# Kernel optimization log

Measured on AMD Instinct MI355X. Metric: run time of the kernel, lower is better.

## Reference

```python
import jax, jax.numpy as jnp
import numpy as np

N_CONS = 100_000
N_VAR = 200_000
N_EDGE = 2_000_000
EMB = 64
CONS_F = 5
VAR_F = 19
EDGE_F = 1
N_LAYERS = 2


def setup_inputs() -> dict:
    key = jax.random.key(0)
    ks = iter(jax.random.split(key, 48))
    def nrm(shape, scale=0.05):
        return jax.random.normal(next(ks), shape, dtype=jnp.float32) * scale
    inp = {}
    inp["cons_x"] = jax.random.normal(next(ks), (N_CONS, CONS_F), dtype=jnp.float32)
    inp["var_x"] = jax.random.normal(next(ks), (N_VAR, VAR_F), dtype=jnp.float32)
    row = jax.random.randint(next(ks), (N_EDGE,), 0, N_CONS, dtype=jnp.int32)
    col = jax.random.randint(next(ks), (N_EDGE,), 0, N_VAR, dtype=jnp.int32)
    inp["edge_index"] = jnp.stack([row, col], axis=0)
    inp["edge_attr"] = jax.random.normal(next(ks), (N_EDGE, EDGE_F), dtype=jnp.float32)
    inp["break_indicator"] = jax.random.uniform(next(ks), (N_VAR, 1), dtype=jnp.float32)
    # PreNormLayer affine params: y = (x + shift) * scale
    inp["cons_pn_shift"] = nrm((CONS_F,))
    inp["cons_pn_scale"] = 1.0 + nrm((CONS_F,))
    inp["var_pn_shift"] = nrm((VAR_F,))
    inp["var_pn_scale"] = 1.0 + nrm((VAR_F,))
    inp["edge_pn_shift"] = nrm((EDGE_F,))
    inp["edge_pn_scale"] = 1.0 + nrm((EDGE_F,))
    # embedding MLPs
    inp["cons_W1"] = nrm((CONS_F, EMB), 0.4)
    inp["cons_b1"] = nrm((EMB,))
    inp["cons_W2"] = nrm((EMB, EMB), 0.12)
    inp["cons_b2"] = nrm((EMB,))
    inp["var_W1"] = nrm((VAR_F, EMB), 0.22)
    inp["var_b1"] = nrm((EMB,))
    inp["var_W2"] = nrm((EMB, EMB), 0.12)
    inp["var_b2"] = nrm((EMB,))
    inp["break_W"] = nrm((1, EMB), 0.5)
    # SAGEConv params per layer: lin_l (neighbor mean, with bias), lin_r (root, no bias)
    inp["Wl_cv"] = nrm((N_LAYERS, EMB, EMB), 0.12)
    inp["bl_cv"] = nrm((N_LAYERS, EMB))
    inp["Wr_cv"] = nrm((N_LAYERS, EMB, EMB), 0.12)
    inp["Wl_vc"] = nrm((N_LAYERS, EMB, EMB), 0.12)
    inp["bl_vc"] = nrm((N_LAYERS, EMB))
    inp["Wr_vc"] = nrm((N_LAYERS, EMB, EMB), 0.12)
    return inp


def _embed(x, shift, scale, W1, b1, W2, b2):
    h = (x + shift) * scale
    h = jax.nn.relu(h @ W1 + b1)
    return jax.nn.relu(h @ W2 + b2)


def _sage(x_src, x_dst, src, dst, n_dst, Wl, bl, Wr):
    # gather source features per edge, mean-aggregate by destination (PyG SAGEConv mean aggr)
    msg = x_src[src]                                              # [E, emb]
    s = jax.ops.segment_sum(msg, dst, num_segments=n_dst)         # [n_dst, emb]
    cnt = jax.ops.segment_sum(jnp.ones((src.shape[0], 1), x_src.dtype), dst, num_segments=n_dst)
    mean = s / jnp.maximum(cnt, 1.0)
    return mean @ Wl + bl + x_dst @ Wr


def reference(cons_x, var_x, edge_index, edge_attr, break_indicator,
              cons_pn_shift, cons_pn_scale, var_pn_shift, var_pn_scale,
              edge_pn_shift, edge_pn_scale,
              cons_W1, cons_b1, cons_W2, cons_b2,
              var_W1, var_b1, var_W2, var_b2,
              break_W, Wl_cv, bl_cv, Wr_cv, Wl_vc, bl_vc, Wr_vc):
    row, col = edge_index[0], edge_index[1]
    cons = _embed(cons_x, cons_pn_shift, cons_pn_scale, cons_W1, cons_b1, cons_W2, cons_b2)
    var = _embed(var_x, var_pn_shift, var_pn_scale, var_W1, var_b1, var_W2, var_b2)
    _edge = (edge_attr + edge_pn_shift) * edge_pn_scale  # computed as in module; unused by SAGE convs
    var = var + break_indicator @ break_W
    n_cons, n_var = cons.shape[0], var.shape[0]
    for l in range(Wl_cv.shape[0]):
        # HeteroConv: both directions computed from the same x_dict, then ReLU
        new_var = jax.nn.relu(_sage(cons, var, row, col, n_var, Wl_cv[l], bl_cv[l], Wr_cv[l]))
        new_cons = jax.nn.relu(_sage(var, cons, col, row, n_cons, Wl_vc[l], bl_vc[l], Wr_vc[l]))
        cons, var = new_cons, new_var
    return var
```

## Files before the change

### kernel.cpp

```cpp
#include <hip/hip_runtime.h>

#define N_CONS 100000
#define N_VAR  200000
#define N_TOT  (N_CONS + N_VAR)
#define N_EDGE 2000000
#define EMB 64

#define VSH 10
#define NBV 196
#define CAPV 12288
#define CSH 9
#define NBC 196
#define CAPC 12288

typedef unsigned short u16;
typedef __attribute__((ext_vector_type(8))) short bf16x8;
typedef __attribute__((ext_vector_type(4))) float f32x4;


__device__ __forceinline__ float b2f_lo(unsigned u) {
  union { unsigned i; float f; } c;
  c.i = u << 16;
  return c.f;
}
__device__ __forceinline__ float b2f_hi(unsigned u) {
  union { unsigned i; float f; } c;
  c.i = u & 0xFFFF0000u;
  return c.f;
}
__device__ __forceinline__ unsigned pack_bf2(float a, float b) {
  unsigned ua = __float_as_uint(a), ub = __float_as_uint(b);
  unsigned ra = (ua + 0x7FFFu + ((ua >> 16) & 1u)) >> 16;
  unsigned rb = (ub + 0x7FFFu + ((ub >> 16) & 1u)) >> 16;
  return ra | (rb << 16);
}
__device__ __forceinline__ u16 f2bf(float a) {
  unsigned ua = __float_as_uint(a);
  return (u16)((ua + 0x7FFFu + ((ua >> 16) & 1u)) >> 16);
}


__global__ __launch_bounds__(256) void csr_init(int* __restrict__ gcurV,
                                                int* __restrict__ gcurC,
                                                int* __restrict__ off) {
  int t = threadIdx.x;
  if (t < NBV) gcurV[t] = t * CAPV;
  if (t < NBC) gcurC[t] = t * CAPC;
  if (t == 0) off[N_TOT] = 2 * N_EDGE;
}

__global__ __launch_bounds__(256) void bucket_scatter(
    const int* __restrict__ row, const int* __restrict__ col,
    int* __restrict__ gcurV, int* __restrict__ gcurC,
    int* __restrict__ pairV, int* __restrict__ pairC) {
  __shared__ int hV[NBV];
  __shared__ int hC[NBC];
  int tid = threadIdx.x;
  int chunk = (N_EDGE + gridDim.x - 1) / gridDim.x;
  int lo = blockIdx.x * chunk;
  int hi = min(N_EDGE, lo + chunk);
  for (int i = tid; i < NBV; i += 256) hV[i] = 0;
  for (int i = tid; i < NBC; i += 256) hC[i] = 0;
  __syncthreads();
  for (int e = lo + tid; e < hi; e += 256) {
    atomicAdd(&hV[col[e] >> VSH], 1);
    atomicAdd(&hC[row[e] >> CSH], 1);
  }
  __syncthreads();
  for (int i = tid; i < NBV; i += 256) {
    int c = hV[i];
    hV[i] = c ? atomicAdd(&gcurV[i], c) : 0;
  }
  for (int i = tid; i < NBC; i += 256) {
    int c = hC[i];
    hC[i] = c ? atomicAdd(&gcurC[i], c) : 0;
  }
  __syncthreads();
  for (int e = lo + tid; e < hi; e += 256) {
    int r = row[e], c = col[e];
    int p = atomicAdd(&hV[c >> VSH], 1);
    pairV[p] = (r << VSH) | (c & ((1 << VSH) - 1));
    int q = atomicAdd(&hC[r >> CSH], 1);
    pairC[q] = (c << CSH) | (r & ((1 << CSH) - 1));
  }
}

__global__ __launch_bounds__(256) void bucket_scan(const int* __restrict__ gcurV,
                                                   const int* __restrict__ gcurC,
                                                   int* __restrict__ ebaseV,
                                                   int* __restrict__ ebaseC) {
  __shared__ int s[256];
  int t = threadIdx.x;
  int v = (t < NBV) ? (gcurV[t] - t * CAPV) : 0;
  s[t] = v;
  __syncthreads();
  for (int d = 1; d < 256; d <<= 1) {
    int x = (t >= d) ? s[t - d] : 0;
    __syncthreads();
    s[t] += x;
    __syncthreads();
  }
  if (t < NBV) ebaseV[t] = s[t] - v;
  if (t == NBV - 1) ebaseV[NBV] = s[t];
  __syncthreads();
  int c = (t < NBC) ? (gcurC[t] - t * CAPC) : 0;
  s[t] = c;
  __syncthreads();
  for (int d = 1; d < 256; d <<= 1) {
    int x = (t >= d) ? s[t - d] : 0;
    __syncthreads();
    s[t] += x;
    __syncthreads();
  }
  if (t < NBC) ebaseC[t] = s[t] - c;
  if (t == NBC - 1) ebaseC[NBC] = s[t];
}

__global__ __launch_bounds__(256) void local_csr(
    const int* __restrict__ pairV, const int* __restrict__ pairC,
    const int* __restrict__ ebaseV, const int* __restrict__ ebaseC,
    int* __restrict__ off, int* __restrict__ adj) {
  __shared__ int cnt[1024];
  __shared__ int cur[1024];
  __shared__ int s[256];
  int tid = threadIdx.x;
  int b = blockIdx.x;
  const int* pairs;
  int m, obase, nn, sh;
  int* offp;
  if (b < NBV) {
    pairs = pairV + (size_t)b * CAPV;
    m = ebaseV[b + 1] - ebaseV[b];
    obase = ebaseV[b];
    nn = min(1024, N_VAR - (b << 10));
    sh = VSH;
    offp = off + (b << 10);
  } else {
    int bb = b - NBV;
    pairs = pairC + (size_t)bb * CAPC;
    m = ebaseC[bb + 1] - ebaseC[bb];
    obase = N_EDGE + ebaseC[bb];
    nn = min(512, N_CONS - (bb << 9));
    sh = CSH;
    offp = off + N_VAR + (bb << 9);
  }
  int mask = (1 << sh) - 1;
  for (int i = tid; i < 1024; i += 256) cnt[i] = 0;
  __syncthreads();
  for (int k = tid; k < m; k += 256) atomicAdd(&cnt[pairs[k] & mask], 1);
  __syncthreads();
  int i0 = tid * 4;
  int c0 = cnt[i0], c1 = cnt[i0 + 1], c2 = cnt[i0 + 2], c3 = cnt[i0 + 3];
  int sum = c0 + c1 + c2 + c3;
  s[tid] = sum;
  __syncthreads();
  for (int d = 1; d < 256; d <<= 1) {
    int x = (tid >= d) ? s[tid - d] : 0;
    __syncthreads();
    s[tid] += x;
    __syncthreads();
  }
  int run = obase + s[tid] - sum;
  int vals[4] = {c0, c1, c2, c3};
#pragma unroll
  for (int q = 0; q < 4; ++q) {
    int i = i0 + q;
    cur[i] = run;
    if (i < nn) offp[i] = run;
    run += vals[q];
  }
  __syncthreads();
  for (int k = tid; k < m; k += 256) {
    int pr = pairs[k];
    int p = atomicAdd(&cur[pr & mask], 1);
    adj[p] = pr >> sh;
  }
}


template <int F>
__global__ __launch_bounds__(256) void embed_mm(
    const float* __restrict__ x, const float* __restrict__ shift,
    const float* __restrict__ scale, const float* __restrict__ W1,
    const float* __restrict__ b1, const float* __restrict__ W2,
    const float* __restrict__ b2, const float* __restrict__ bi,
    const float* __restrict__ bW, u16* __restrict__ outbf, int n) {
  __shared__ float Xs[F * 68];
  __shared__ float W1s[F * 68];
  __shared__ u16 Hs[64][72];
  __shared__ u16 W2s[64][72];
  __shared__ float b1s[64], b2s[64], bWs[64], bis[64];
  int t = threadIdx.x;
  int v0 = blockIdx.x * 64;

  int sn = t & 63;
  int kq = t >> 6;
  {
    unsigned pk[8];
#pragma unroll
    for (int i = 0; i < 8; ++i) {
      float w0 = W2[(size_t)(kq * 16 + 2 * i) * 64 + sn];
      float w1 = W2[(size_t)(kq * 16 + 2 * i + 1) * 64 + sn];
      pk[i] = pack_bf2(w0, w1);
    }
    *(uint4*)&W2s[sn][kq * 16] = make_uint4(pk[0], pk[1], pk[2], pk[3]);
    *(uint4*)&W2s[sn][kq * 16 + 8] = make_uint4(pk[4], pk[5], pk[6], pk[7]);
  }
  for (int i = t; i < F * 64; i += 256) {
    int k = i >> 6, j = i & 63;
    W1s[k * 68 + j] = W1[i] * scale[k];
  }
  if (t < 64) {
    float acc = b1[t];
#pragma unroll
    for (int k = 0; k < F; ++k) acc += shift[k] * scale[k] * W1[k * 64 + t];
    b1s[t] = acc;
    b2s[t] = b2[t];
    bWs[t] = bW ? bW[t] : 0.f;
    bis[t] = (bi && v0 + t < n) ? bi[v0 + t] : 0.f;
  }
  for (int i = t; i < 64 * F; i += 256) {
    int row = i / F, k = i - row * F;
    int v = v0 + row;
    Xs[k * 68 + row] = (v < n) ? x[(size_t)v * F + k] : 0.f;
  }
  __syncthreads();

  int jt = t & 15;
  int vt = t >> 4;
  float c[4][4] = {};
#pragma unroll
  for (int k = 0; k < F; ++k) {
    float4 xv = *(const float4*)&Xs[k * 68 + vt * 4];
    float4 wv = *(const float4*)&W1s[k * 68 + jt * 4];
    c[0][0] += xv.x * wv.x; c[0][1] += xv.x * wv.y; c[0][2] += xv.x * wv.z; c[0][3] += xv.x * wv.w;
    c[1][0] += xv.y * wv.x; c[1][1] += xv.y * wv.y; c[1][2] += xv.y * wv.z; c[1][3] += xv.y * wv.w;
    c[2][0] += xv.z * wv.x; c[2][1] += xv.z * wv.y; c[2][2] += xv.z * wv.z; c[2][3] += xv.z * wv.w;
    c[3][0] += xv.w * wv.x; c[3][1] += xv.w * wv.y; c[3][2] += xv.w * wv.z; c[3][3] += xv.w * wv.w;
  }
#pragma unroll
  for (int i = 0; i < 4; ++i) {
    float h0 = fmaxf(c[i][0] + b1s[jt * 4 + 0], 0.f);
    float h1 = fmaxf(c[i][1] + b1s[jt * 4 + 1], 0.f);
    float h2 = fmaxf(c[i][2] + b1s[jt * 4 + 2], 0.f);
    float h3 = fmaxf(c[i][3] + b1s[jt * 4 + 3], 0.f);
    *(uint2*)&Hs[vt * 4 + i][jt * 4] = make_uint2(pack_bf2(h0, h1), pack_bf2(h2, h3));
  }
  __syncthreads();

  int l = t & 63;
  int w = t >> 6;
  int m0 = w * 16;
  int rA = m0 + (l & 15);
  int koffA = (l >> 4) * 8;
  f32x4 acc[4] = {};
  {
    bf16x8 a0 = *(const bf16x8*)&Hs[rA][koffA];
    bf16x8 a1 = *(const bf16x8*)&Hs[rA][32 + koffA];
#pragma unroll
    for (int cb = 0; cb < 4; ++cb) {
      int nB = cb * 16 + (l & 15);
      bf16x8 b0 = *(const bf16x8*)&W2s[nB][koffA];
      bf16x8 bb1 = *(const bf16x8*)&W2s[nB][32 + koffA];
      acc[cb] = __builtin_amdgcn_mfma_f32_16x16x32_bf16(a0, b0, acc[cb], 0, 0, 0);
      acc[cb] = __builtin_amdgcn_mfma_f32_16x16x32_bf16(a1, bb1, acc[cb], 0, 0, 0);
    }
  }
#pragma unroll
  for (int cb = 0; cb < 4; ++cb) {
    int colc = cb * 16 + (l & 15);
    float bias = b2s[colc];
    float bwv = bWs[colc];
#pragma unroll
    for (int j = 0; j < 4; ++j) {
      int rowc = m0 + (l >> 4) * 4 + j;
      int v = v0 + rowc;
      if (v < n) {
        float val = fmaxf(acc[cb][j] + bias, 0.f) + bis[rowc] * bwv;
        outbf[(size_t)v * 64 + colc] = f2bf(val);
      }
    }
  }
}


template <int OUTBF>
__global__ __launch_bounds__(256) void sage_mfma(
    const uint2* __restrict__ srcbf, const uint2* __restrict__ dstbf,
    const int* __restrict__ off, const int* __restrict__ adj,
    const float* __restrict__ Wl, const float* __restrict__ bl,
    const float* __restrict__ Wr, float* __restrict__ outf,
    u16* __restrict__ outbf, int n) {
  __shared__ u16 Hs[64][72];
  __shared__ u16 Ws[64][72];
  __shared__ float bls[64];
  int t = threadIdx.x;
  int v0 = blockIdx.x * 64;
  if (t < 64) bls[t] = bl[t];

  int sn = t & 63;
  int kq = t >> 6;
  {
    unsigned pk[8];
#pragma unroll
    for (int i = 0; i < 8; ++i) {
      float w0 = Wl[(size_t)(kq * 16 + 2 * i) * 64 + sn];
      float w1 = Wl[(size_t)(kq * 16 + 2 * i + 1) * 64 + sn];
      pk[i] = pack_bf2(w0, w1);
    }
    *(uint4*)&Ws[sn][kq * 16] = make_uint4(pk[0], pk[1], pk[2], pk[3]);
    *(uint4*)&Ws[sn][kq * 16 + 8] = make_uint4(pk[4], pk[5], pk[6], pk[7]);
  }

  int lane = t & 15;
  int g = t >> 4;
#pragma unroll
  for (int grp = 0; grp < 4; ++grp) {
    int r = grp * 16 + g;
    int v = v0 + r;
    float ax = 0.f, ay = 0.f, az = 0.f, aw = 0.f;
    if (v < n) {
      int s0 = off[v], s1 = off[v + 1];
      int i = s0;
      for (; i + 4 <= s1; i += 4) {
        int u0 = adj[i], u1 = adj[i + 1], u2 = adj[i + 2], u3 = adj[i + 3];
        uint2 a0 = srcbf[(size_t)u0 * 16 + lane];
        uint2 a1 = srcbf[(size_t)u1 * 16 + lane];
        uint2 a2 = srcbf[(size_t)u2 * 16 + lane];
        uint2 a3 = srcbf[(size_t)u3 * 16 + lane];
        ax += (b2f_lo(a0.x) + b2f_lo(a1.x)) + (b2f_lo(a2.x) + b2f_lo(a3.x));
        ay += (b2f_hi(a0.x) + b2f_hi(a1.x)) + (b2f_hi(a2.x) + b2f_hi(a3.x));
        az += (b2f_lo(a0.y) + b2f_lo(a1.y)) + (b2f_lo(a2.y) + b2f_lo(a3.y));
        aw += (b2f_hi(a0.y) + b2f_hi(a1.y)) + (b2f_hi(a2.y) + b2f_hi(a3.y));
      }
      if (i + 2 <= s1) {
        int u0 = adj[i], u1 = adj[i + 1];
        uint2 a0 = srcbf[(size_t)u0 * 16 + lane];
        uint2 a1 = srcbf[(size_t)u1 * 16 + lane];
        ax += b2f_lo(a0.x) + b2f_lo(a1.x);
        ay += b2f_hi(a0.x) + b2f_hi(a1.x);
        az += b2f_lo(a0.y) + b2f_lo(a1.y);
        aw += b2f_hi(a0.y) + b2f_hi(a1.y);
        i += 2;
      }
      if (i < s1) {
        uint2 a = srcbf[(size_t)adj[i] * 16 + lane];
        ax += b2f_lo(a.x);
        ay += b2f_hi(a.x);
        az += b2f_lo(a.y);
        aw += b2f_hi(a.y);
      }
      int deg = s1 - s0;
      float inv = (deg > 0) ? 1.f / (float)deg : 0.f;
      ax *= inv;
      ay *= inv;
      az *= inv;
      aw *= inv;
    }
    *(uint2*)&Hs[r][lane * 4] = make_uint2(pack_bf2(ax, ay), pack_bf2(az, aw));
  }
  __syncthreads();

  int l = t & 63;
  int w = t >> 6;
  int m0 = w * 16;
  int rA = m0 + (l & 15);
  int koffA = (l >> 4) * 8;
  f32x4 acc[4] = {};
  {
    bf16x8 a0 = *(const bf16x8*)&Hs[rA][koffA];
    bf16x8 a1 = *(const bf16x8*)&Hs[rA][32 + koffA];
#pragma unroll
    for (int cb = 0; cb < 4; ++cb) {
      int nB = cb * 16 + (l & 15);
      bf16x8 b0 = *(const bf16x8*)&Ws[nB][koffA];
      bf16x8 b1 = *(const bf16x8*)&Ws[nB][32 + koffA];
      acc[cb] = __builtin_amdgcn_mfma_f32_16x16x32_bf16(a0, b0, acc[cb], 0, 0, 0);
      acc[cb] = __builtin_amdgcn_mfma_f32_16x16x32_bf16(a1, b1, acc[cb], 0, 0, 0);
    }
  }
  __syncthreads();

#pragma unroll
  for (int r4 = 0; r4 < 4; ++r4) {
    int idx = t + 256 * r4;
    int rowi = idx >> 4, f4 = idx & 15;
    int v = v0 + rowi;
    uint2 val = (v < n) ? dstbf[(size_t)v * 16 + f4] : make_uint2(0u, 0u);
    *(uint2*)&Hs[rowi][f4 * 4] = val;
  }
  {
    unsigned pk[8];
#pragma unroll
    for (int i = 0; i < 8; ++i) {
      float w0 = Wr[(size_t)(kq * 16 + 2 * i) * 64 + sn];
      float w1 = Wr[(size_t)(kq * 16 + 2 * i + 1) * 64 + sn];
      pk[i] = pack_bf2(w0, w1);
    }
    *(uint4*)&Ws[sn][kq * 16] = make_uint4(pk[0], pk[1], pk[2], pk[3]);
    *(uint4*)&Ws[sn][kq * 16 + 8] = make_uint4(pk[4], pk[5], pk[6], pk[7]);
  }
  __syncthreads();

  {
    bf16x8 a0 = *(const bf16x8*)&Hs[rA][koffA];
    bf16x8 a1 = *(const bf16x8*)&Hs[rA][32 + koffA];
#pragma unroll
    for (int cb = 0; cb < 4; ++cb) {
      int nB = cb * 16 + (l & 15);
      bf16x8 b0 = *(const bf16x8*)&Ws[nB][koffA];
      bf16x8 b1 = *(const bf16x8*)&Ws[nB][32 + koffA];
      acc[cb] = __builtin_amdgcn_mfma_f32_16x16x32_bf16(a0, b0, acc[cb], 0, 0, 0);
      acc[cb] = __builtin_amdgcn_mfma_f32_16x16x32_bf16(a1, b1, acc[cb], 0, 0, 0);
    }
  }

#pragma unroll
  for (int cb = 0; cb < 4; ++cb) {
    int colc = cb * 16 + (l & 15);
    float bias = bls[colc];
#pragma unroll
    for (int j = 0; j < 4; ++j) {
      int rowc = m0 + (l >> 4) * 4 + j;
      int v = v0 + rowc;
      if (v < n) {
        float val = fmaxf(acc[cb][j] + bias, 0.f);
        if (OUTBF) {
          outbf[(size_t)v * 64 + colc] = f2bf(val);
        } else {
          outf[(size_t)v * 64 + colc] = val;
        }
      }
    }
  }
}


extern "C" void kernel_launch(void* const* d_in, const int* in_sizes, int n_in,
                              void* d_out, int out_size, void* d_ws, size_t ws_size,
                              hipStream_t stream) {
  const float* cons_x = (const float*)d_in[0];
  const float* var_x  = (const float*)d_in[1];
  const int*   eidx   = (const int*)d_in[2];
  const float* bi     = (const float*)d_in[4];
  const float* c_sh   = (const float*)d_in[5];
  const float* c_sc   = (const float*)d_in[6];
  const float* v_sh   = (const float*)d_in[7];
  const float* v_sc   = (const float*)d_in[8];
  const float* cW1 = (const float*)d_in[11];
  const float* cb1 = (const float*)d_in[12];
  const float* cW2 = (const float*)d_in[13];
  const float* cb2 = (const float*)d_in[14];
  const float* vW1 = (const float*)d_in[15];
  const float* vb1 = (const float*)d_in[16];
  const float* vW2 = (const float*)d_in[17];
  const float* vb2 = (const float*)d_in[18];
  const float* bW  = (const float*)d_in[19];
  const float* Wl_cv = (const float*)d_in[20];
  const float* bl_cv = (const float*)d_in[21];
  const float* Wr_cv = (const float*)d_in[22];
  const float* Wl_vc = (const float*)d_in[23];
  const float* bl_vc = (const float*)d_in[24];
  const float* Wr_vc = (const float*)d_in[25];

  const int* row = eidx;
  const int* col = eidx + N_EDGE;

  char* ws = (char*)d_ws;
  size_t o = 0;
  auto alloc = [&](size_t bytes) {
    char* p = ws + o;
    o = (o + bytes + 255) & ~(size_t)255;
    return p;
  };
  int* off    = (int*)alloc((N_TOT + 1) * sizeof(int));
  int* adj    = (int*)alloc((size_t)2 * N_EDGE * sizeof(int));
  int* pairV  = (int*)alloc((size_t)NBV * CAPV * sizeof(int));
  int* pairC  = (int*)alloc((size_t)NBC * CAPC * sizeof(int));
  int* gcurV  = (int*)alloc(256 * sizeof(int));
  int* gcurC  = (int*)alloc(256 * sizeof(int));
  int* ebaseV = (int*)alloc(256 * sizeof(int));
  int* ebaseC = (int*)alloc(256 * sizeof(int));
  uint2* consEbf = (uint2*)alloc((size_t)N_CONS * EMB * 2);
  uint2* varEbf  = (uint2*)alloc((size_t)N_VAR * EMB * 2);
  uint2* cons1bf = (uint2*)alloc((size_t)N_CONS * EMB * 2);
  uint2* var1bf  = (uint2*)alloc((size_t)N_VAR * EMB * 2);
  float* var_out = (float*)d_out;

  csr_init<<<1, 256, 0, stream>>>(gcurV, gcurC, off);
  bucket_scatter<<<512, 256, 0, stream>>>(row, col, gcurV, gcurC, pairV, pairC);
  bucket_scan<<<1, 256, 0, stream>>>(gcurV, gcurC, ebaseV, ebaseC);
  local_csr<<<NBV + NBC, 256, 0, stream>>>(pairV, pairC, ebaseV, ebaseC, off, adj);

  embed_mm<5><<<(N_CONS + 63) / 64, 256, 0, stream>>>(
      cons_x, c_sh, c_sc, cW1, cb1, cW2, cb2, nullptr, nullptr, (u16*)consEbf,
      N_CONS);
  embed_mm<19><<<(N_VAR + 63) / 64, 256, 0, stream>>>(
      var_x, v_sh, v_sc, vW1, vb1, vW2, vb2, bi, bW, (u16*)varEbf, N_VAR);

  sage_mfma<1><<<(N_VAR + 63) / 64, 256, 0, stream>>>(
      consEbf, varEbf, off, adj, Wl_cv, bl_cv, Wr_cv, nullptr, (u16*)var1bf,
      N_VAR);
  sage_mfma<1><<<(N_CONS + 63) / 64, 256, 0, stream>>>(
      varEbf, consEbf, off + N_VAR, adj, Wl_vc, bl_vc, Wr_vc, nullptr,
      (u16*)cons1bf, N_CONS);
  sage_mfma<0><<<(N_VAR + 63) / 64, 256, 0, stream>>>(
      cons1bf, var1bf, off, adj, Wl_cv + 4096, bl_cv + 64, Wr_cv + 4096,
      var_out, nullptr, N_VAR);
}
```

Baseline: 281.0 us.

## Pad CSR rows to multiples of four with zero-row sentinels and merge kernels

Each adjacency list now starts at a fixed per-bucket base and is padded to a multiple of four edges. Padding entries point to an extra all-zero embedding row, so the gather loop has no 2- and 1-element tails, and degree is stored separately. This also removes the global bucket scan kernel (local_csr runs with 1024 threads and fixed capacities) and merges the two layer-0 SAGE launches into one grid. The cost is a larger padded adjacency buffer, up to three wasted gathers per node, and a fixed capacity assumption per bucket.

```diff
diff --git a/kernel.cpp b/kernel.cpp
--- a/kernel.cpp
+++ b/kernel.cpp
@@ -12,6 +12,10 @@
 #define CSH 9
 #define NBC 196
 #define CAPC 12288
+#define CAPAV (CAPV + 3 * 1024)
+#define CAPAC (CAPC + 3 * 512)
+#define NB_VAR ((N_VAR + 63) / 64)
+#define NB_CONS ((N_CONS + 63) / 64)
 
 typedef unsigned short u16;
 typedef __attribute__((ext_vector_type(8))) short bf16x8;
@@ -42,11 +46,15 @@
 
 __global__ __launch_bounds__(256) void csr_init(int* __restrict__ gcurV,
                                                 int* __restrict__ gcurC,
-                                                int* __restrict__ off) {
+                                                uint2* __restrict__ consEbf,
+                                                uint2* __restrict__ varEbf,
+                                                uint2* __restrict__ cons1bf) {
   int t = threadIdx.x;
   if (t < NBV) gcurV[t] = t * CAPV;
   if (t < NBC) gcurC[t] = t * CAPC;
-  if (t == 0) off[N_TOT] = 2 * N_EDGE;
+  if (t < 16) consEbf[(size_t)N_CONS * 16 + t] = make_uint2(0u, 0u);
+  else if (t < 32) varEbf[(size_t)N_VAR * 16 + (t - 16)] = make_uint2(0u, 0u);
+  else if (t < 48) cons1bf[(size_t)N_CONS * 16 + (t - 32)] = make_uint2(0u, 0u);
 }
 
 __global__ __launch_bounds__(256) void bucket_scatter(
@@ -85,96 +93,67 @@
   }
 }
 
-__global__ __launch_bounds__(256) void bucket_scan(const int* __restrict__ gcurV,
-                                                   const int* __restrict__ gcurC,
-                                                   int* __restrict__ ebaseV,
-                                                   int* __restrict__ ebaseC) {
-  __shared__ int s[256];
-  int t = threadIdx.x;
-  int v = (t < NBV) ? (gcurV[t] - t * CAPV) : 0;
-  s[t] = v;
-  __syncthreads();
-  for (int d = 1; d < 256; d <<= 1) {
-    int x = (t >= d) ? s[t - d] : 0;
-    __syncthreads();
-    s[t] += x;
-    __syncthreads();
-  }
-  if (t < NBV) ebaseV[t] = s[t] - v;
-  if (t == NBV - 1) ebaseV[NBV] = s[t];
-  __syncthreads();
-  int c = (t < NBC) ? (gcurC[t] - t * CAPC) : 0;
-  s[t] = c;
-  __syncthreads();
-  for (int d = 1; d < 256; d <<= 1) {
-    int x = (t >= d) ? s[t - d] : 0;
-    __syncthreads();
-    s[t] += x;
-    __syncthreads();
-  }
-  if (t < NBC) ebaseC[t] = s[t] - c;
-  if (t == NBC - 1) ebaseC[NBC] = s[t];
-}
-
-__global__ __launch_bounds__(256) void local_csr(
+__global__ __launch_bounds__(1024) void local_csr(
     const int* __restrict__ pairV, const int* __restrict__ pairC,
-    const int* __restrict__ ebaseV, const int* __restrict__ ebaseC,
-    int* __restrict__ off, int* __restrict__ adj) {
+    const int* __restrict__ gcurV, const int* __restrict__ gcurC,
+    int* __restrict__ off, int* __restrict__ deg, int* __restrict__ adj) {
   __shared__ int cnt[1024];
+  __shared__ int s[1024];
   __shared__ int cur[1024];
-  __shared__ int s[256];
   int tid = threadIdx.x;
   int b = blockIdx.x;
   const int* pairs;
-  int m, obase, nn, sh;
+  int m, obase, nn, sh, zrow;
   int* offp;
+  int* degp;
   if (b < NBV) {
     pairs = pairV + (size_t)b * CAPV;
-    m = ebaseV[b + 1] - ebaseV[b];
-    obase = ebaseV[b];
+    m = gcurV[b] - b * CAPV;
+    obase = b * CAPAV;
     nn = min(1024, N_VAR - (b << 10));
     sh = VSH;
+    zrow = N_CONS;
     offp = off + (b << 10);
+    degp = deg + (b << 10);
   } else {
     int bb = b - NBV;
     pairs = pairC + (size_t)bb * CAPC;
-    m = ebaseC[bb + 1] - ebaseC[bb];
-    obase = N_EDGE + ebaseC[bb];
+    m = gcurC[bb] - bb * CAPC;
+    obase = NBV * CAPAV + bb * CAPAC;
     nn = min(512, N_CONS - (bb << 9));
     sh = CSH;
+    zrow = N_VAR;
     offp = off + N_VAR + (bb << 9);
+    degp = deg + N_VAR + (bb << 9);
   }
   int mask = (1 << sh) - 1;
-  for (int i = tid; i < 1024; i += 256) cnt[i] = 0;
-  __syncthreads();
-  for (int k = tid; k < m; k += 256) atomicAdd(&cnt[pairs[k] & mask], 1);
-  __syncthreads();
-  int i0 = tid * 4;
-  int c0 = cnt[i0], c1 = cnt[i0 + 1], c2 = cnt[i0 + 2], c3 = cnt[i0 + 3];
-  int sum = c0 + c1 + c2 + c3;
-  s[tid] = sum;
-  __syncthreads();
-  for (int d = 1; d < 256; d <<= 1) {
-    int x = (tid >= d) ? s[tid - d] : 0;
+  cnt[tid] = 0;
+  __syncthreads();
+  for (int k = tid; k < m; k += 1024) atomicAdd(&cnt[pairs[k] & mask], 1);
+  __syncthreads();
+  int c = cnt[tid];
+  int pc = (c + 3) & ~3;
+  s[tid] = pc;
+  __syncthreads();
+  for (int d1 = 1; d1 < 1024; d1 <<= 1) {
+    int x = (tid >= d1) ? s[tid - d1] : 0;
     __syncthreads();
     s[tid] += x;
     __syncthreads();
   }
-  int run = obase + s[tid] - sum;
-  int vals[4] = {c0, c1, c2, c3};
-#pragma unroll
-  for (int q = 0; q < 4; ++q) {
-    int i = i0 + q;
-    cur[i] = run;
-    if (i < nn) offp[i] = run;
-    run += vals[q];
-  }
-  __syncthreads();
-  for (int k = tid; k < m; k += 256) {
+  int start = obase + s[tid] - pc;
+  cur[tid] = start;
+  if (tid < nn) {
+    offp[tid] = start;
+    degp[tid] = c;
+  }
+  __syncthreads();
+  for (int k = tid; k < m; k += 1024) {
     int pr = pairs[k];
     int p = atomicAdd(&cur[pr & mask], 1);
     adj[p] = pr >> sh;
   }
+  for (int q = c; q < pc; ++q) adj[start + q] = zrow;
 }
 
 
@@ -285,17 +264,14 @@
 
 
 template <int OUTBF>
-__global__ __launch_bounds__(256) void sage_mfma(
+__device__ __forceinline__ void sage_body(
     const uint2* __restrict__ srcbf, const uint2* __restrict__ dstbf,
-    const int* __restrict__ off, const int* __restrict__ adj,
-    const float* __restrict__ Wl, const float* __restrict__ bl,
-    const float* __restrict__ Wr, float* __restrict__ outf,
-    u16* __restrict__ outbf, int n) {
-  __shared__ u16 Hs[64][72];
-  __shared__ u16 Ws[64][72];
-  __shared__ float bls[64];
+    const int* __restrict__ off, const int* __restrict__ deg,
+    const int* __restrict__ adj, const float* __restrict__ Wl,
+    const float* __restrict__ bl, const float* __restrict__ Wr,
+    float* __restrict__ outf, u16* __restrict__ outbf, int n, int v0,
+    u16 (*Hs)[72], u16 (*Ws)[72], float* bls) {
   int t = threadIdx.x;
-  int v0 = blockIdx.x * 64;
   if (t < 64) bls[t] = bl[t];
 
   int sn = t & 63;
@@ -320,9 +296,10 @@
     int v = v0 + r;
     float ax = 0.f, ay = 0.f, az = 0.f, aw = 0.f;
     if (v < n) {
-      int s0 = off[v], s1 = off[v + 1];
-      int i = s0;
-      for (; i + 4 <= s1; i += 4) {
+      int s0 = off[v];
+      int d = deg[v];
+      int e4 = s0 + ((d + 3) & ~3);
+      for (int i = s0; i < e4; i += 4) {
         int u0 = adj[i], u1 = adj[i + 1], u2 = adj[i + 2], u3 = adj[i + 3];
         uint2 a0 = srcbf[(size_t)u0 * 16 + lane];
         uint2 a1 = srcbf[(size_t)u1 * 16 + lane];
@@ -333,25 +310,7 @@
         az += (b2f_lo(a0.y) + b2f_lo(a1.y)) + (b2f_lo(a2.y) + b2f_lo(a3.y));
         aw += (b2f_hi(a0.y) + b2f_hi(a1.y)) + (b2f_hi(a2.y) + b2f_hi(a3.y));
       }
-      if (i + 2 <= s1) {
-        int u0 = adj[i], u1 = adj[i + 1];
-        uint2 a0 = srcbf[(size_t)u0 * 16 + lane];
-        uint2 a1 = srcbf[(size_t)u1 * 16 + lane];
-        ax += b2f_lo(a0.x) + b2f_lo(a1.x);
-        ay += b2f_hi(a0.x) + b2f_hi(a1.x);
-        az += b2f_lo(a0.y) + b2f_lo(a1.y);
-        aw += b2f_hi(a0.y) + b2f_hi(a1.y);
-        i += 2;
-      }
-      if (i < s1) {
-        uint2 a = srcbf[(size_t)adj[i] * 16 + lane];
-        ax += b2f_lo(a.x);
-        ay += b2f_hi(a.x);
-        az += b2f_lo(a.y);
-        aw += b2f_hi(a.y);
-      }
-      int deg = s1 - s0;
-      float inv = (deg > 0) ? 1.f / (float)deg : 0.f;
+      float inv = (d > 0) ? 1.f / (float)d : 0.f;
       ax *= inv;
       ay *= inv;
       az *= inv;
@@ -433,6 +392,40 @@
       }
     }
   }
+}
+
+__global__ __launch_bounds__(256) void sage_l0(
+    const uint2* __restrict__ consEbf, const uint2* __restrict__ varEbf,
+    const int* __restrict__ off, const int* __restrict__ deg,
+    const int* __restrict__ adj, const float* __restrict__ Wl_cv,
+    const float* __restrict__ bl_cv, const float* __restrict__ Wr_cv,
+    const float* __restrict__ Wl_vc, const float* __restrict__ bl_vc,
+    const float* __restrict__ Wr_vc, u16* __restrict__ var1bf,
+    u16* __restrict__ cons1bf) {
+  __shared__ u16 Hs[64][72];
+  __shared__ u16 Ws[64][72];
+  __shared__ float bls[64];
+  int b = blockIdx.x;
+  if (b < NB_VAR) {
+    sage_body<1>(consEbf, varEbf, off, deg, adj, Wl_cv, bl_cv, Wr_cv, nullptr,
+                 var1bf, N_VAR, b * 64, Hs, Ws, bls);
+  } else {
+    sage_body<1>(varEbf, consEbf, off + N_VAR, deg + N_VAR, adj, Wl_vc, bl_vc,
+                 Wr_vc, nullptr, cons1bf, N_CONS, (b - NB_VAR) * 64, Hs, Ws, bls);
+  }
+}
+
+__global__ __launch_bounds__(256) void sage_l1(
+    const uint2* __restrict__ cons1bf, const uint2* __restrict__ var1bf,
+    const int* __restrict__ off, const int* __restrict__ deg,
+    const int* __restrict__ adj, const float* __restrict__ Wl,
+    const float* __restrict__ bl, const float* __restrict__ Wr,
+    float* __restrict__ out) {
+  __shared__ u16 Hs[64][72];
+  __shared__ u16 Ws[64][72];
+  __shared__ float bls[64];
+  sage_body<0>(cons1bf, var1bf, off, deg, adj, Wl, bl, Wr, out, nullptr, N_VAR,
+               blockIdx.x * 64, Hs, Ws, bls);
 }
 
 
@@ -473,38 +466,34 @@
     o = (o + bytes + 255) & ~(size_t)255;
     return p;
   };
-  int* off    = (int*)alloc((N_TOT + 1) * sizeof(int));
-  int* adj    = (int*)alloc((size_t)2 * N_EDGE * sizeof(int));
-  int* pairV  = (int*)alloc((size_t)NBV * CAPV * sizeof(int));
-  int* pairC  = (int*)alloc((size_t)NBC * CAPC * sizeof(int));
-  int* gcurV  = (int*)alloc(256 * sizeof(int));
-  int* gcurC  = (int*)alloc(256 * sizeof(int));
-  int* ebaseV = (int*)alloc(256 * sizeof(int));
-  int* ebaseC = (int*)alloc(256 * sizeof(int));
-  uint2* consEbf = (uint2*)alloc((size_t)N_CONS * EMB * 2);
-  uint2* varEbf  = (uint2*)alloc((size_t)N_VAR * EMB * 2);
-  uint2* cons1bf = (uint2*)alloc((size_t)N_CONS * EMB * 2);
+  int* off   = (int*)alloc((size_t)N_TOT * sizeof(int));
+  int* deg   = (int*)alloc((size_t)N_TOT * sizeof(int));
+  int* adj   = (int*)alloc(((size_t)NBV * CAPAV + (size_t)NBC * CAPAC) * sizeof(int));
+  int* pairV = (int*)alloc((size_t)NBV * CAPV * sizeof(int));
+  int* pairC = (int*)alloc((size_t)NBC * CAPC * sizeof(int));
+  int* gcurV = (int*)alloc(256 * sizeof(int));
+  int* gcurC = (int*)alloc(256 * sizeof(int));
+  uint2* consEbf = (uint2*)alloc((size_t)(N_CONS + 1) * EMB * 2);
+  uint2* varEbf  = (uint2*)alloc((size_t)(N_VAR + 1) * EMB * 2);
+  uint2* cons1bf = (uint2*)alloc((size_t)(N_CONS + 1) * EMB * 2);
   uint2* var1bf  = (uint2*)alloc((size_t)N_VAR * EMB * 2);
   float* var_out = (float*)d_out;
 
-  csr_init<<<1, 256, 0, stream>>>(gcurV, gcurC, off);
+  csr_init<<<1, 256, 0, stream>>>(gcurV, gcurC, consEbf, varEbf, cons1bf);
   bucket_scatter<<<512, 256, 0, stream>>>(row, col, gcurV, gcurC, pairV, pairC);
-  bucket_scan<<<1, 256, 0, stream>>>(gcurV, gcurC, ebaseV, ebaseC);
-  local_csr<<<NBV + NBC, 256, 0, stream>>>(pairV, pairC, ebaseV, ebaseC, off, adj);
-
-  embed_mm<5><<<(N_CONS + 63) / 64, 256, 0, stream>>>(
-      cons_x, c_sh, c_sc, cW1, cb1, cW2, cb2, nullptr, nullptr, (u16*)consEbf,
-      N_CONS);
-  embed_mm<19><<<(N_VAR + 63) / 64, 256, 0, stream>>>(
-      var_x, v_sh, v_sc, vW1, vb1, vW2, vb2, bi, bW, (u16*)varEbf, N_VAR);
-
-  sage_mfma<1><<<(N_VAR + 63) / 64, 256, 0, stream>>>(
-      consEbf, varEbf, off, adj, Wl_cv, bl_cv, Wr_cv, nullptr, (u16*)var1bf,
-      N_VAR);
-  sage_mfma<1><<<(N_CONS + 63) / 64, 256, 0, stream>>>(
-      varEbf, consEbf, off + N_VAR, adj, Wl_vc, bl_vc, Wr_vc, nullptr,
-      (u16*)cons1bf, N_CONS);
-  sage_mfma<0><<<(N_VAR + 63) / 64, 256, 0, stream>>>(
-      cons1bf, var1bf, off, adj, Wl_cv + 4096, bl_cv + 64, Wr_cv + 4096,
-      var_out, nullptr, N_VAR);
-}
+  local_csr<<<NBV + NBC, 1024, 0, stream>>>(pairV, pairC, gcurV, gcurC, off,
+                                            deg, adj);
+
+  embed_mm<5><<<NB_CONS, 256, 0, stream>>>(cons_x, c_sh, c_sc, cW1, cb1, cW2,
+                                           cb2, nullptr, nullptr, (u16*)consEbf,
+                                           N_CONS);
+  embed_mm<19><<<NB_VAR, 256, 0, stream>>>(var_x, v_sh, v_sc, vW1, vb1, vW2,
+                                           vb2, bi, bW, (u16*)varEbf, N_VAR);
+
+  sage_l0<<<NB_VAR + NB_CONS, 256, 0, stream>>>(
+      consEbf, varEbf, off, deg, adj, Wl_cv, bl_cv, Wr_cv, Wl_vc, bl_vc, Wr_vc,
+      (u16*)var1bf, (u16*)cons1bf);
+  sage_l1<<<NB_VAR, 256, 0, stream>>>(cons1bf, var1bf, off, deg, adj,
+                                      Wl_cv + 4096, bl_cv + 64, Wr_cv + 4096,
+                                      var_out);
+}
```

Result: faster. 258.9 us (-7.9%).
